# Kernel optimization log

Hardware: AMD Instinct MI355X
Metric: run time of the kernel (lower is better)

## Reference

```python
import jax, jax.numpy as jnp
import numpy as np

B, T, D = 2, 2048, 1024
H = 16
HD = D // H
SCALE = 1.0 / np.sqrt(HD).astype(np.float32)


def setup_inputs() -> dict:
    key = jax.random.key(0)
    ks = jax.random.split(key, 5)
    std = 1.0 / np.sqrt(D).astype(np.float32)
    x = jax.random.normal(ks[0], (B, T, D), dtype=jnp.float32)
    Wqkvt = jax.random.normal(ks[1], (D, 4 * D), dtype=jnp.float32) * std
    bqkvt = jax.random.normal(ks[2], (4 * D,), dtype=jnp.float32) * 0.02
    Wout = jax.random.normal(ks[3], (D, D), dtype=jnp.float32) * std
    bout = jax.random.normal(ks[4], (D,), dtype=jnp.float32) * 0.02
    return {"x": x, "Wqkvt": Wqkvt, "bqkvt": bqkvt, "Wout": Wout, "bout": bout}


def reference(x, Wqkvt, bqkvt, Wout, bout):
    b, t, d = x.shape
    # fused qkvt projection -> [B,T,4,H,HD]
    qkvt = (x @ Wqkvt + bqkvt).reshape(b, t, 4, H, HD)
    # -> [B,H,T,HD] each
    q, k, v, tt = [jnp.transpose(qkvt[:, :, i], (0, 2, 1, 3)) for i in range(4)]

    # standard dot-product scores [B,H,T,T]
    scores_dot = jnp.einsum('bhqd,bhkd->bhqk', q, k)
    # triplet term: (q*t) against cumsum over keys of (k*v)/sqrt(hd)
    kv = k * v * SCALE
    kv_cum = jnp.cumsum(kv, axis=2)  # causal prefix over key positions
    scores_trip = jnp.einsum('bhqd,bhkd->bhqk', q * tt, kv_cum)

    scores = (scores_dot + scores_trip) * SCALE
    causal = jnp.triu(jnp.ones((t, t), dtype=bool), k=1)
    scores = jnp.where(causal[None, None], -jnp.inf, scores)

    attn = jax.nn.softmax(scores, axis=-1)
    out = jnp.einsum('bhqk,bhkd->bhqd', attn, v)  # [B,H,T,HD]
    out = jnp.transpose(out, (0, 2, 1, 3)).reshape(b, t, d)
    return out @ Wout + bout
```

## Files before the change

kernel.cpp:

```cpp
#include <hip/hip_runtime.h>

#define T_SEQ 2048
#define D_MODEL 1024
#define NH 16
#define HD 64
#define BH_TOT 32
#define M_ROWS 4096
#define NT 32
#define SCALE 0.125f
#define BHT (BH_TOT * T_SEQ)
#define LOG2E 1.44269504f
#define TAU 2.885f

typedef _Float16 h8 __attribute__((ext_vector_type(8)));
typedef _Float16 h4 __attribute__((ext_vector_type(4)));
typedef float f32x4 __attribute__((ext_vector_type(4)));

__device__ __forceinline__ f32x4 mfma_h(h8 a, h8 b, f32x4 c) {
    return __builtin_amdgcn_mfma_f32_16x16x32_f16(a, b, c, 0, 0, 0);
}

__global__ void k_convert(const float* __restrict__ in, _Float16* __restrict__ out, int n) {
    int i = (blockIdx.x * blockDim.x + threadIdx.x) * 4;
    if (i < n) {
        float4 v = *(const float4*)(in + i);
        h4 o;
        o[0] = (_Float16)v.x; o[1] = (_Float16)v.y;
        o[2] = (_Float16)v.z; o[3] = (_Float16)v.w;
        *(h4*)(out + i) = o;
    }
}

__global__ void k_transpose(const float* __restrict__ in, _Float16* __restrict__ out, int K, int N) {
    __shared__ float tile[32][33];
    int nb = blockIdx.x * 32, kb = blockIdx.y * 32;
    int tx = threadIdx.x & 31, ty = threadIdx.x >> 5;
    #pragma unroll
    for (int i = 0; i < 32; i += 8)
        tile[ty + i][tx] = in[(size_t)(kb + ty + i) * N + (nb + tx)];
    __syncthreads();
    #pragma unroll
    for (int i = 0; i < 32; i += 8)
        out[(size_t)(nb + ty + i) * K + (kb + tx)] = (_Float16)tile[tx][ty + i];
}

template<int MODE>
__launch_bounds__(256, 2)
__global__ void k_gemm(const _Float16* __restrict__ A, const _Float16* __restrict__ Bt,
                       int M, int N, int K, const float* __restrict__ bias,
                       _Float16* __restrict__ qo, _Float16* __restrict__ keo,
                       _Float16* __restrict__ vo, _Float16* __restrict__ vto,
                       _Float16* __restrict__ to, float* __restrict__ cOut)
{
    constexpr int LDT = 40;
    __shared__ __align__(16) _Float16 lA[128 * LDT];
    __shared__ __align__(16) _Float16 lB[128 * LDT];
    const int tid = threadIdx.x;
    const int wid = tid >> 6, lane = tid & 63, lrow = lane & 15, lg = lane >> 4;
    const int wm = wid >> 1, wn = wid & 1;
    const int m0 = blockIdx.x * 128, n0 = blockIdx.y * 128;

    f32x4 acc[4][4];
    #pragma unroll
    for (int i = 0; i < 4; i++)
        #pragma unroll
        for (int j = 0; j < 4; j++) acc[i][j] = (f32x4){0.f, 0.f, 0.f, 0.f};

    const int srow = tid >> 1, scol = (tid & 1) * 16;
    const _Float16* ga = A + (size_t)(m0 + srow) * K + scol;
    const _Float16* gb = Bt + (size_t)(n0 + srow) * K + scol;

    h8 ra0 = *(const h8*)ga, ra1 = *(const h8*)(ga + 8);
    h8 rb0 = *(const h8*)gb, rb1 = *(const h8*)(gb + 8);
    const int nk = K / 32;
    for (int kt = 0; kt < nk; ++kt) {
        *(h8*)&lA[srow * LDT + scol]     = ra0;
        *(h8*)&lA[srow * LDT + scol + 8] = ra1;
        *(h8*)&lB[srow * LDT + scol]     = rb0;
        *(h8*)&lB[srow * LDT + scol + 8] = rb1;
        __syncthreads();
        if (kt + 1 < nk) {
            ra0 = *(const h8*)(ga + (kt + 1) * 32);
            ra1 = *(const h8*)(ga + (kt + 1) * 32 + 8);
            rb0 = *(const h8*)(gb + (kt + 1) * 32);
            rb1 = *(const h8*)(gb + (kt + 1) * 32 + 8);
        }
        h8 af[4], bfr[4];
        #pragma unroll
        for (int mi = 0; mi < 4; mi++)
            af[mi] = *(const h8*)&lA[(wm * 64 + mi * 16 + lrow) * LDT + lg * 8];
        #pragma unroll
        for (int ni = 0; ni < 4; ni++)
            bfr[ni] = *(const h8*)&lB[(wn * 64 + ni * 16 + lrow) * LDT + lg * 8];
        #pragma unroll
        for (int mi = 0; mi < 4; mi++)
            #pragma unroll
            for (int ni = 0; ni < 4; ni++)
                acc[mi][ni] = mfma_h(af[mi], bfr[ni], acc[mi][ni]);
        __syncthreads();
    }

    if (MODE == 0) {
        const int ssel = n0 >> 10;
        #pragma unroll
        for (int mi = 0; mi < 4; mi++) {
            #pragma unroll
            for (int ni = 0; ni < 4; ni++) {
                const int nn = n0 + wn * 64 + ni * 16 + lrow;
                const float bv = bias[nn];
                const int h = (nn >> 6) & 15, hd = nn & 63;
                #pragma unroll
                for (int r = 0; r < 4; r++) {
                    const int mm = m0 + wm * 64 + mi * 16 + 4 * lg + r;
                    const int b = mm >> 11, t = mm & (T_SEQ - 1);
                    const _Float16 hv = (_Float16)(acc[mi][ni][r] + bv);
                    const size_t row = (size_t)(b * NH + h) * T_SEQ + t;
                    if (ssel == 0) qo[row * HD + hd] = hv;
                    else if (ssel == 1) keo[row * 128 + hd] = hv;
                    else if (ssel == 2) {
                        vo[row * HD + hd] = hv;
                        vto[((size_t)(b * NH + h) * HD + hd) * T_SEQ + t] = hv;
                    } else to[row * HD + hd] = hv;
                }
            }
        }
    } else {
        #pragma unroll
        for (int mi = 0; mi < 4; mi++) {
            #pragma unroll
            for (int ni = 0; ni < 4; ni++) {
                const int nn = n0 + wn * 64 + ni * 16 + lrow;
                const float bv = bias[nn];
                #pragma unroll
                for (int r = 0; r < 4; r++) {
                    const int mm = m0 + wm * 64 + mi * 16 + 4 * lg + r;
                    cOut[(size_t)mm * N + nn] = acc[mi][ni][r] + bv;
                }
            }
        }
    }
}

__global__ void k_kvcum(_Float16* __restrict__ Ke, const _Float16* __restrict__ Vb)
{
    const int bh = blockIdx.x;
    const int w = threadIdx.x >> 6, lane = threadIdx.x & 63;
    const size_t bk = (size_t)bh * T_SEQ * 128 + lane;
    const size_t bv = (size_t)bh * T_SEQ * HD + lane;
    const int CH = T_SEQ / 16;
    const int t0 = w * CH;
    float s = 0.f;
    for (int i = 0; i < CH; i++)
        s += (float)Ke[bk + (size_t)(t0 + i) * 128] * (float)Vb[bv + (size_t)(t0 + i) * HD];
    __shared__ float tot[16][64];
    tot[w][lane] = s;
    __syncthreads();
    float acc = 0.f;
    for (int ww = 0; ww < w; ww++) acc += tot[ww][lane];
    for (int i = 0; i < CH; i++) {
        size_t ok = bk + (size_t)(t0 + i) * 128;
        acc += (float)Ke[ok] * (float)Vb[bv + (size_t)(t0 + i) * HD];
        Ke[ok + 64] = (_Float16)(acc * SCALE);
    }
}

__launch_bounds__(256, 4)
__global__ void k_attn(const _Float16* __restrict__ Qb, const _Float16* __restrict__ Ke,
                       const _Float16* __restrict__ Vt, const _Float16* __restrict__ Tb,
                       _Float16* __restrict__ Op0, _Float16* __restrict__ Op1,
                       _Float16* __restrict__ Op2, _Float16* __restrict__ Op3,
                       float* __restrict__ ML, int nsplit)
{
    const int bh = blockIdx.x;
    const int pair = blockIdx.y;
    const int ksel = blockIdx.z;
    const int tid = threadIdx.x;
    const int wid = tid >> 6, lane = tid & 63, lrow = lane & 15, lg = lane >> 4;
    const _Float16* qp = Qb + (size_t)bh * T_SEQ * HD;
    const _Float16* kep = Ke + (size_t)bh * T_SEQ * 128;
    const _Float16* tp = Tb + (size_t)bh * T_SEQ * HD;
    const _Float16* vp = Vt + (size_t)bh * T_SEQ * HD;
    _Float16* op = (ksel == 0) ? Op0 : (ksel == 1) ? Op1 : (ksel == 2) ? Op2 : Op3;
    float* ml = ML + (size_t)ksel * BHT * 2;

    __shared__ __align__(16) _Float16 ldsK[64 * 128];
    __shared__ __align__(16) _Float16 ldsV[64 * 64];
    __shared__ __align__(16) _Float16 lP[4][16 * 64];

    const int kpos = tid & 15, kprow = tid >> 4;
    const int vpos = tid & 7,  vprow = tid >> 3;
    const int r7 = lrow & 7;
    int kswz[4];
    #pragma unroll
    for (int c = 0; c < 4; c++) kswz[c] = ((c * 4 + lg) ^ r7) * 8;

    const h8 ones = {(_Float16)1.f, (_Float16)1.f, (_Float16)1.f, (_Float16)1.f,
                     (_Float16)1.f, (_Float16)1.f, (_Float16)1.f, (_Float16)1.f};
    const float C = SCALE * LOG2E;

    for (int half = 0; half < 2; ++half) {
        const int qi = half ? (NT - 1 - pair) : pair;
        const int q0 = qi * 64;
        const int nj = qi + 1;
        const int jbeg = (nj * ksel) / nsplit;
        const int jend = (nj * (ksel + 1)) / nsplit;

        const int qrow = q0 + wid * 16 + lrow;
        h8 qf[4];
        #pragma unroll
        for (int ks = 0; ks < 2; ++ks) {
            h8 qv = *(const h8*)&qp[(size_t)qrow * HD + ks * 32 + lg * 8];
            h8 tv = *(const h8*)&tp[(size_t)qrow * HD + ks * 32 + lg * 8];
            h8 a2, b2;
            #pragma unroll
            for (int i = 0; i < 8; i++) {
                float qq = (float)qv[i] * C;
                a2[i] = (_Float16)qq;
                b2[i] = (_Float16)(qq * (float)tv[i]);
            }
            qf[ks] = a2; qf[2 + ks] = b2;
        }

        float m_r[4];
        f32x4 o[4], o4;
        #pragma unroll
        for (int r = 0; r < 4; r++) m_r[r] = -__builtin_inff();
        #pragma unroll
        for (int ct = 0; ct < 4; ct++) o[ct] = (f32x4){0.f, 0.f, 0.f, 0.f};
        o4 = (f32x4){0.f, 0.f, 0.f, 0.f};

        for (int j = jbeg; j < jend; ++j) {
            __syncthreads();
            #pragma unroll
            for (int rr = 0; rr < 4; rr++) {
                const int row = rr * 16 + kprow;
                h8 kv = *(const h8*)&kep[(size_t)(j * 64 + row) * 128 + kpos * 8];
                *(h8*)&ldsK[row * 128 + ((kpos ^ (row & 7)) * 8)] = kv;
            }
            #pragma unroll
            for (int rr = 0; rr < 2; rr++) {
                const int d = rr * 32 + vprow;
                h8 vv = *(const h8*)&vp[(size_t)d * T_SEQ + j * 64 + vpos * 8];
                *(h8*)&ldsV[d * 64 + ((vpos ^ (d & 7)) * 8)] = vv;
            }
            __syncthreads();

            f32x4 s[4];
            #pragma unroll
            for (int ct = 0; ct < 4; ct++) {
                const _Float16* kb = &ldsK[(ct * 16 + lrow) * 128];
                f32x4 sv = (f32x4){0.f, 0.f, 0.f, 0.f};
                sv = mfma_h(qf[0], *(const h8*)&kb[kswz[0]], sv);
                sv = mfma_h(qf[1], *(const h8*)&kb[kswz[1]], sv);
                sv = mfma_h(qf[2], *(const h8*)&kb[kswz[2]], sv);
                sv = mfma_h(qf[3], *(const h8*)&kb[kswz[3]], sv);
                s[ct] = sv;
            }
            if (j == qi) {
                #pragma unroll
                for (int ct = 0; ct < 4; ct++)
                    #pragma unroll
                    for (int r = 0; r < 4; r++) {
                        int key = j * 64 + ct * 16 + lrow;
                        int qr  = q0 + wid * 16 + 4 * lg + r;
                        if (key > qr) s[ct][r] = -__builtin_inff();
                    }
            }
            float mx[4];
            #pragma unroll
            for (int r = 0; r < 4; r++)
                mx[r] = fmaxf(fmaxf(s[0][r], s[1][r]), fmaxf(s[2][r], s[3][r]));
            bool need = (mx[0] > m_r[0] + TAU) | (mx[1] > m_r[1] + TAU) |
                        (mx[2] > m_r[2] + TAU) | (mx[3] > m_r[3] + TAU);
            if (__any(need)) {
                #pragma unroll
                for (int d = 1; d < 16; d <<= 1)
                    #pragma unroll
                    for (int r = 0; r < 4; r++) mx[r] = fmaxf(mx[r], __shfl_xor(mx[r], d, 64));
                #pragma unroll
                for (int r = 0; r < 4; r++) {
                    float mn = fmaxf(m_r[r], mx[r]);
                    float scl = __builtin_amdgcn_exp2f(m_r[r] - mn);
                    o[0][r] *= scl; o[1][r] *= scl; o[2][r] *= scl; o[3][r] *= scl;
                    o4[r] *= scl;
                    m_r[r] = mn;
                }
            }
            #pragma unroll
            for (int ct = 0; ct < 4; ct++) {
                const int col = ct * 16 + lrow;
                #pragma unroll
                for (int r = 0; r < 4; r++) {
                    float p = __builtin_amdgcn_exp2f(s[ct][r] - m_r[r]);
                    const int row = 4 * lg + r;
                    const int boff = row * 128 + ((col * 2) ^ ((row & 7) << 4));
                    lP[wid][boff >> 1] = (_Float16)p;
                }
            }
            h8 pa[2];
            #pragma unroll
            for (int ks = 0; ks < 2; ks++) {
                const int boff = lrow * 128 + ((ks * 64 + lg * 16) ^ ((lrow & 7) << 4));
                pa[ks] = *(const h8*)((const char*)lP[wid] + boff);
            }
            o4 = mfma_h(pa[0], ones, o4);
            o4 = mfma_h(pa[1], ones, o4);
            #pragma unroll
            for (int ct = 0; ct < 4; ct++) {
                const _Float16* vb = &ldsV[(ct * 16 + lrow) * 64];
                o[ct] = mfma_h(pa[0], *(const h8*)&vb[kswz[0]], o[ct]);
                o[ct] = mfma_h(pa[1], *(const h8*)&vb[kswz[1]], o[ct]);
            }
        }
        #pragma unroll
        for (int ct = 0; ct < 4; ct++)
            #pragma unroll
            for (int r = 0; r < 4; r++) {
                const int trow = q0 + wid * 16 + 4 * lg + r;
                const int d = ct * 16 + lrow;
                op[((size_t)bh * T_SEQ + trow) * HD + d] = (_Float16)o[ct][r];
            }
        if (lrow == 0) {
            #pragma unroll
            for (int r = 0; r < 4; r++) {
                const int trow = q0 + wid * 16 + 4 * lg + r;
                const size_t mi = ((size_t)bh * T_SEQ + trow) * 2;
                ml[mi] = m_r[r];
                ml[mi + 1] = o4[r];
            }
        }
    }
}

__global__ void k_combine(const _Float16* __restrict__ Op0, const _Float16* __restrict__ Op1,
                          const _Float16* __restrict__ Op2, const _Float16* __restrict__ Op3,
                          const float* __restrict__ ML, _Float16* __restrict__ AO, int nsplit)
{
    const int idx = blockIdx.x * 256 + threadIdx.x;
    const int row = idx >> 3;
    const int d0 = (idx & 7) * 8;
    const int bh = row >> 11, t = row & (T_SEQ - 1);
    const int b = bh >> 4, h = bh & 15;
    const _Float16* ops[4] = {Op0, Op1, Op2, Op3};
    float m = -__builtin_inff();
    for (int c = 0; c < nsplit; c++) m = fmaxf(m, ML[(size_t)c * BHT * 2 + 2 * row]);
    float w[4], denom = 0.f;
    for (int c = 0; c < nsplit; c++) {
        w[c] = __builtin_amdgcn_exp2f(ML[(size_t)c * BHT * 2 + 2 * row] - m);
        denom += w[c] * ML[(size_t)c * BHT * 2 + 2 * row + 1];
    }
    const float inv = 1.0f / denom;
    float accv[8];
    #pragma unroll
    for (int i = 0; i < 8; i++) accv[i] = 0.f;
    for (int c = 0; c < nsplit; c++) {
        h8 a = *(const h8*)&ops[c][(size_t)row * HD + d0];
        #pragma unroll
        for (int i = 0; i < 8; i++) accv[i] += w[c] * (float)a[i];
    }
    h8 r;
    #pragma unroll
    for (int i = 0; i < 8; i++) r[i] = (_Float16)(accv[i] * inv);
    *(h8*)&AO[((size_t)(b * T_SEQ + t)) * D_MODEL + h * HD + d0] = r;
}

extern "C" void kernel_launch(void* const* d_in, const int* in_sizes, int n_in,
                              void* d_out, int out_size, void* d_ws, size_t ws_size,
                              hipStream_t stream)
{
    const float* x     = (const float*)d_in[0];
    const float* Wqkvt = (const float*)d_in[1];
    const float* bqkvt = (const float*)d_in[2];
    const float* Wout  = (const float*)d_in[3];
    const float* bout  = (const float*)d_in[4];
    float* out = (float*)d_out;

    char* ws = (char*)d_ws;
    size_t off = 0;
    auto alloc = [&](size_t bytes) {
        char* p = ws + off;
        off += (bytes + 255) & ~(size_t)255;
        return p;
    };
    const size_t SZ = (size_t)M_ROWS * D_MODEL * 2;
    _Float16* xb  = (_Float16*)alloc(SZ);
    _Float16* wt  = (_Float16*)alloc(SZ);
    _Float16* wo  = (_Float16*)alloc((size_t)D_MODEL * D_MODEL * 2);
    _Float16* Qh  = (_Float16*)alloc(SZ);
    _Float16* Ke  = (_Float16*)alloc(SZ * 2);
    _Float16* Vh  = (_Float16*)alloc(SZ);
    _Float16* Vth = (_Float16*)alloc(SZ);
    _Float16* Th  = (_Float16*)alloc(SZ);
    _Float16* AO  = (_Float16*)alloc(SZ);
    const size_t need4 = off + 2 * SZ;
    _Float16* Op2 = (_Float16*)alloc(SZ);
    _Float16* Op3 = (_Float16*)alloc(SZ);

    const int nsplit = (ws_size >= need4) ? 4 : 2;

    _Float16* Op0 = xb;
    _Float16* Op1 = Vh;
    float*    ML  = (float*)wt;

    k_convert<<<4096, 256, 0, stream>>>(x, xb, M_ROWS * D_MODEL);
    k_transpose<<<dim3(128, 32), 256, 0, stream>>>(Wqkvt, wt, D_MODEL, 4 * D_MODEL);
    k_transpose<<<dim3(32, 32), 256, 0, stream>>>(Wout, wo, D_MODEL, D_MODEL);
    k_gemm<0><<<dim3(32, 32), 256, 0, stream>>>(xb, wt, M_ROWS, 4 * D_MODEL, D_MODEL,
                                                bqkvt, Qh, Ke, Vh, Vth, Th, nullptr);
    k_kvcum<<<BH_TOT, 1024, 0, stream>>>(Ke, Vh);
    k_attn<<<dim3(BH_TOT, NT / 2, nsplit), 256, 0, stream>>>(Qh, Ke, Vth, Th,
                                                             Op0, Op1, Op2, Op3, ML, nsplit);
    k_combine<<<BHT * HD / 8 / 256, 256, 0, stream>>>(Op0, Op1, Op2, Op3, ML, AO, nsplit);
    k_gemm<1><<<dim3(32, 8), 256, 0, stream>>>(AO, wo, M_ROWS, D_MODEL, D_MODEL,
                                               bout, nullptr, nullptr, nullptr, nullptr,
                                               nullptr, out);
}
```

Measured before the change: 190.5 us.

## Use direct global-to-LDS loads in GEMM and prefetch K/V tiles in attention

The GEMM now loads 64-wide K tiles straight into LDS through global_load_lds, with an XOR swizzle in place of padding, and issues two MFMAs per fragment pair. This drops the register staging but also the previous register prefetch, so load latency is no longer overlapped with compute. The attention loop register-prefetches the next K/V tile while the current one is computed, and the QKV epilogue writes the transposed V as h4 vectors. Correctness depends on the swizzled global_load_lds addressing matching the LDS layout the readers expect.

```diff
diff --git a/kernel.cpp b/kernel.cpp
--- a/kernel.cpp
+++ b/kernel.cpp
@@ -20,6 +20,12 @@
     return __builtin_amdgcn_mfma_f32_16x16x32_f16(a, b, c, 0, 0, 0);
 }
 
+__device__ __forceinline__ void gload16(const _Float16* g, _Float16* l) {
+    __builtin_amdgcn_global_load_lds(
+        (const __attribute__((address_space(1))) unsigned int*)g,
+        (__attribute__((address_space(3))) unsigned int*)l, 16, 0, 0);
+}
+
 __global__ void k_convert(const float* __restrict__ in, _Float16* __restrict__ out, int n) {
     int i = (blockIdx.x * blockDim.x + threadIdx.x) * 4;
     if (i < n) {
@@ -52,9 +58,8 @@
                        _Float16* __restrict__ vo, _Float16* __restrict__ vto,
                        _Float16* __restrict__ to, float* __restrict__ cOut)
 {
-    constexpr int LDT = 40;
-    __shared__ __align__(16) _Float16 lA[128 * LDT];
-    __shared__ __align__(16) _Float16 lB[128 * LDT];
+    __shared__ __align__(16) _Float16 lA[128 * 64];
+    __shared__ __align__(16) _Float16 lB[128 * 64];
     const int tid = threadIdx.x;
     const int wid = tid >> 6, lane = tid & 63, lrow = lane & 15, lg = lane >> 4;
     const int wm = wid >> 1, wn = wid & 1;
@@ -66,37 +71,44 @@
         #pragma unroll
         for (int j = 0; j < 4; j++) acc[i][j] = (f32x4){0.f, 0.f, 0.f, 0.f};
 
-    const int srow = tid >> 1, scol = (tid & 1) * 16;
-    const _Float16* ga = A + (size_t)(m0 + srow) * K + scol;
-    const _Float16* gb = Bt + (size_t)(n0 + srow) * K + scol;
-
-    h8 ra0 = *(const h8*)ga, ra1 = *(const h8*)(ga + 8);
-    h8 rb0 = *(const h8*)gb, rb1 = *(const h8*)(gb + 8);
-    const int nk = K / 32;
+    const int rin = lane >> 3, gcol = lane & 7;
+    const int scol = (gcol ^ rin) * 8;
+    const _Float16* gA = A + (size_t)(m0 + 32 * wid + rin) * K + scol;
+    const _Float16* gB = Bt + (size_t)(n0 + 32 * wid + rin) * K + scol;
+    _Float16* lAw = &lA[32 * wid * 64];
+    _Float16* lBw = &lB[32 * wid * 64];
+
+    const int r7 = lrow & 7;
+    const int nk = K >> 6;
     for (int kt = 0; kt < nk; ++kt) {
-        *(h8*)&lA[srow * LDT + scol]     = ra0;
-        *(h8*)&lA[srow * LDT + scol + 8] = ra1;
-        *(h8*)&lB[srow * LDT + scol]     = rb0;
-        *(h8*)&lB[srow * LDT + scol + 8] = rb1;
+        const size_t ko = (size_t)kt * 64;
+        #pragma unroll
+        for (int i = 0; i < 4; i++) {
+            gload16(gA + (size_t)(8 * i) * K + ko, lAw + 8 * i * 64);
+            gload16(gB + (size_t)(8 * i) * K + ko, lBw + 8 * i * 64);
+        }
         __syncthreads();
-        if (kt + 1 < nk) {
-            ra0 = *(const h8*)(ga + (kt + 1) * 32);
-            ra1 = *(const h8*)(ga + (kt + 1) * 32 + 8);
-            rb0 = *(const h8*)(gb + (kt + 1) * 32);
-            rb1 = *(const h8*)(gb + (kt + 1) * 32 + 8);
-        }
-        h8 af[4], bfr[4];
+
+        h8 af[4][2], bfr[4][2];
+        #pragma unroll
+        for (int mi = 0; mi < 4; mi++) {
+            const int row = wm * 64 + mi * 16 + lrow;
+            af[mi][0] = *(const h8*)&lA[row * 64 + ((lg ^ r7) * 8)];
+            af[mi][1] = *(const h8*)&lA[row * 64 + (((4 + lg) ^ r7) * 8)];
+        }
+        #pragma unroll
+        for (int ni = 0; ni < 4; ni++) {
+            const int row = wn * 64 + ni * 16 + lrow;
+            bfr[ni][0] = *(const h8*)&lB[row * 64 + ((lg ^ r7) * 8)];
+            bfr[ni][1] = *(const h8*)&lB[row * 64 + (((4 + lg) ^ r7) * 8)];
+        }
         #pragma unroll
         for (int mi = 0; mi < 4; mi++)
-            af[mi] = *(const h8*)&lA[(wm * 64 + mi * 16 + lrow) * LDT + lg * 8];
-        #pragma unroll
-        for (int ni = 0; ni < 4; ni++)
-            bfr[ni] = *(const h8*)&lB[(wn * 64 + ni * 16 + lrow) * LDT + lg * 8];
-        #pragma unroll
-        for (int mi = 0; mi < 4; mi++)
-            #pragma unroll
-            for (int ni = 0; ni < 4; ni++)
-                acc[mi][ni] = mfma_h(af[mi], bfr[ni], acc[mi][ni]);
+            #pragma unroll
+            for (int ni = 0; ni < 4; ni++) {
+                acc[mi][ni] = mfma_h(af[mi][0], bfr[ni][0], acc[mi][ni]);
+                acc[mi][ni] = mfma_h(af[mi][1], bfr[ni][1], acc[mi][ni]);
+            }
         __syncthreads();
     }
 
@@ -109,18 +121,25 @@
                 const int nn = n0 + wn * 64 + ni * 16 + lrow;
                 const float bv = bias[nn];
                 const int h = (nn >> 6) & 15, hd = nn & 63;
-                #pragma unroll
-                for (int r = 0; r < 4; r++) {
-                    const int mm = m0 + wm * 64 + mi * 16 + 4 * lg + r;
-                    const int b = mm >> 11, t = mm & (T_SEQ - 1);
-                    const _Float16 hv = (_Float16)(acc[mi][ni][r] + bv);
-                    const size_t row = (size_t)(b * NH + h) * T_SEQ + t;
-                    if (ssel == 0) qo[row * HD + hd] = hv;
-                    else if (ssel == 1) keo[row * 128 + hd] = hv;
-                    else if (ssel == 2) {
-                        vo[row * HD + hd] = hv;
-                        vto[((size_t)(b * NH + h) * HD + hd) * T_SEQ + t] = hv;
-                    } else to[row * HD + hd] = hv;
+                const int mmb = m0 + wm * 64 + mi * 16 + 4 * lg;
+                const int b = mmb >> 11, t0 = mmb & (T_SEQ - 1);
+                const size_t rowb = (size_t)(b * NH + h) * T_SEQ;
+                h4 hv;
+                #pragma unroll
+                for (int r = 0; r < 4; r++) hv[r] = (_Float16)(acc[mi][ni][r] + bv);
+                if (ssel == 0) {
+                    #pragma unroll
+                    for (int r = 0; r < 4; r++) qo[(rowb + t0 + r) * HD + hd] = hv[r];
+                } else if (ssel == 1) {
+                    #pragma unroll
+                    for (int r = 0; r < 4; r++) keo[(rowb + t0 + r) * 128 + hd] = hv[r];
+                } else if (ssel == 2) {
+                    #pragma unroll
+                    for (int r = 0; r < 4; r++) vo[(rowb + t0 + r) * HD + hd] = hv[r];
+                    *(h4*)&vto[((size_t)(b * NH + h) * HD + hd) * T_SEQ + t0] = hv;
+                } else {
+                    #pragma unroll
+                    for (int r = 0; r < 4; r++) to[(rowb + t0 + r) * HD + hd] = hv[r];
                 }
             }
         }
@@ -229,21 +248,31 @@
         for (int ct = 0; ct < 4; ct++) o[ct] = (f32x4){0.f, 0.f, 0.f, 0.f};
         o4 = (f32x4){0.f, 0.f, 0.f, 0.f};
 
+        h8 stK[4], stV[2];
+        auto issue = [&](int j) {
+            #pragma unroll
+            for (int rr = 0; rr < 4; rr++)
+                stK[rr] = *(const h8*)&kep[(size_t)(j * 64 + rr * 16 + kprow) * 128 + kpos * 8];
+            #pragma unroll
+            for (int rr = 0; rr < 2; rr++)
+                stV[rr] = *(const h8*)&vp[(size_t)(rr * 32 + vprow) * T_SEQ + j * 64 + vpos * 8];
+        };
+        if (jbeg < jend) issue(jbeg);
+
         for (int j = jbeg; j < jend; ++j) {
             __syncthreads();
             #pragma unroll
             for (int rr = 0; rr < 4; rr++) {
                 const int row = rr * 16 + kprow;
-                h8 kv = *(const h8*)&kep[(size_t)(j * 64 + row) * 128 + kpos * 8];
-                *(h8*)&ldsK[row * 128 + ((kpos ^ (row & 7)) * 8)] = kv;
+                *(h8*)&ldsK[row * 128 + ((kpos ^ (row & 7)) * 8)] = stK[rr];
             }
             #pragma unroll
             for (int rr = 0; rr < 2; rr++) {
                 const int d = rr * 32 + vprow;
-                h8 vv = *(const h8*)&vp[(size_t)d * T_SEQ + j * 64 + vpos * 8];
-                *(h8*)&ldsV[d * 64 + ((vpos ^ (d & 7)) * 8)] = vv;
+                *(h8*)&ldsV[d * 64 + ((vpos ^ (d & 7)) * 8)] = stV[rr];
             }
             __syncthreads();
+            if (j + 1 < jend) issue(j + 1);
 
             f32x4 s[4];
             #pragma unroll
```

New measurement: 191.4 us. Within noise of the previous version (+0.5%).
